# Optimization experiments

Measured on AMD Instinct MI355X. Metric: run time of the kernel, lower is better.

## Reference

```python
import jax, jax.numpy as jnp
import numpy as np

N_HEAD = 16
N_KV_HEAD = 8
HEAD_DIM = 128
N_EMBED = 2048
EPS = 1.1920929e-07  # torch default eps for fp32 rms_norm


def _apply_rotary_emb(x, cos, sin):
    # x: (B, T, H, D); cos/sin: (1, T, 1, D//2)  (nanochat-style half rotation)
    d = x.shape[-1] // 2
    x1, x2 = x[..., :d], x[..., d:]
    y1 = x1 * cos + x2 * sin
    y2 = -x1 * sin + x2 * cos
    return jnp.concatenate([y1, y2], axis=-1).astype(x.dtype)


def _rms_norm(x):
    return x * jax.lax.rsqrt(jnp.mean(jnp.square(x), axis=-1, keepdims=True) + EPS)


def setup_inputs() -> dict:
    key = jax.random.key(0)
    ks = jax.random.split(key, 5)
    B, T = 2, 2048
    kv_dim = N_KV_HEAD * HEAD_DIM
    x = jax.random.normal(ks[0], (B, T, N_EMBED), dtype=jnp.float32)
    w_attn = jax.random.normal(ks[1], (N_EMBED + 2 * kv_dim, N_EMBED), dtype=jnp.float32) * 0.02
    w_proj = jax.random.normal(ks[2], (N_EMBED, N_EMBED), dtype=jnp.float32) * 0.02
    # realistic RoPE tables
    half = HEAD_DIM // 2
    inv_freq = 1.0 / (10000.0 ** (jnp.arange(half, dtype=jnp.float32) / half))
    freqs = jnp.arange(T, dtype=jnp.float32)[:, None] * inv_freq[None, :]  # (T, half)
    cos = jnp.cos(freqs)[None, :, None, :]
    sin = jnp.sin(freqs)[None, :, None, :]
    return {"x": x, "w_attn": w_attn, "w_proj": w_proj, "cos": cos, "sin": sin}


def reference(x, w_attn, w_proj, cos, sin):
    B, T, C = x.shape
    kv_dim = N_KV_HEAD * HEAD_DIM
    qkv = jnp.einsum('btc,oc->bto', x, w_attn)  # (B, T, C + 2*kv_dim)
    q = qkv[..., :C].reshape(B, T, N_HEAD, HEAD_DIM)
    k = qkv[..., C:C + kv_dim].reshape(B, T, N_KV_HEAD, HEAD_DIM)
    v = qkv[..., C + kv_dim:].reshape(B, T, N_KV_HEAD, HEAD_DIM)
    q = _rms_norm(_apply_rotary_emb(q, cos, sin))
    k = _rms_norm(_apply_rotary_emb(k, cos, sin))
    # GQA: repeat kv heads to match query heads
    rep = N_HEAD // N_KV_HEAD
    k = jnp.repeat(k, rep, axis=2)  # (B, T, n_head, D)
    v = jnp.repeat(v, rep, axis=2)
    scale = 1.0 / jnp.sqrt(jnp.float32(HEAD_DIM))
    scores = jnp.einsum('bqhd,bkhd->bhqk', q, k) * scale  # (B, H, T, T)
    causal = jnp.tril(jnp.ones((T, T), dtype=bool))
    scores = jnp.where(causal[None, None], scores, jnp.finfo(scores.dtype).min)
    attn = jax.nn.softmax(scores, axis=-1)
    y = jnp.einsum('bhqk,bkhd->bqhd', attn, v).reshape(B, T, C)
    return jnp.einsum('btc,oc->bto', y, w_proj)
```

## Files before the change

kernel.cpp:

```cpp
#include <hip/hip_runtime.h>

#define B_ 2
#define T_ 2048
#define NH 16
#define NKV 8
#define HD 128
#define C_ 2048
#define KVD (NKV*HD)
#define QKVD (C_ + 2*KVD)
#define NTOK (B_*T_)

typedef __bf16 bf16_t;
typedef __bf16 bf16x2_t __attribute__((ext_vector_type(2)));
typedef __bf16 bf16x4_t __attribute__((ext_vector_type(4)));
typedef __bf16 bf16x8_t __attribute__((ext_vector_type(8)));
typedef float f32x4_t __attribute__((ext_vector_type(4)));
typedef float f32x16_t __attribute__((ext_vector_type(16)));
typedef int i32x4_t __attribute__((ext_vector_type(4)));

__device__ __forceinline__ f32x4_t mfma16(bf16x8_t a, bf16x8_t b, f32x4_t c) {
  return __builtin_amdgcn_mfma_f32_16x16x32_bf16(a, b, c, 0, 0, 0);
}
__device__ __forceinline__ f32x16_t mfma32(bf16x8_t a, bf16x8_t b, f32x16_t c) {
  return __builtin_amdgcn_mfma_f32_32x32x16_bf16(a, b, c, 0, 0, 0);
}
__device__ __forceinline__ f32x16_t zero16() {
  f32x16_t z;
  #pragma unroll
  for (int i = 0; i < 16; i++) z[i] = 0.f;
  return z;
}
__device__ __forceinline__ int pk2(float a, float b) {
  bf16x2_t t; t[0] = (bf16_t)a; t[1] = (bf16_t)b;
  return __builtin_bit_cast(int, t);
}

#define GLDS16(gp, lp) __builtin_amdgcn_global_load_lds( \
    (const __attribute__((address_space(1))) void*)(gp), \
    (__attribute__((address_space(3))) void*)(lp), 16, 0, 0)

__global__ __launch_bounds__(256) void cvt3_kernel(const float* __restrict__ s0, bf16_t* __restrict__ d0,
                                                   const float* __restrict__ s1, bf16_t* __restrict__ d1,
                                                   const float* __restrict__ s2, bf16_t* __restrict__ d2) {
  int bid = blockIdx.x;
  const float* s; bf16_t* d; int off;
  if (bid < 8192)       { s = s0; d = d0; off = bid; }
  else if (bid < 16384) { s = s1; d = d1; off = bid - 8192; }
  else                  { s = s2; d = d2; off = bid - 16384; }
  int i = (off * 256 + threadIdx.x) * 4;
  const float4 v = *(const float4*)(s + i);
  bf16x4_t o;
  o[0] = (bf16_t)v.x; o[1] = (bf16_t)v.y; o[2] = (bf16_t)v.z; o[3] = (bf16_t)v.w;
  *(bf16x4_t*)(d + i) = o;
}

template<int BM>
__global__ __launch_bounds__(512, 1) void gemm_nt2(const bf16_t* __restrict__ A,
                                                   const bf16_t* __restrict__ Bm,
                                                   float* __restrict__ Cf, bf16_t* __restrict__ Cb,
                                                   int M, int N, int K) {
  constexpr int MR = BM / 32;
  constexpr int RA = BM / 64;
  __shared__ __align__(16) bf16_t As[2][BM * 64];
  __shared__ __align__(16) bf16_t Bs[2][256 * 64];
  int tid = threadIdx.x;
  int wave = tid >> 6, lane = tid & 63;
  int quad = lane >> 4, l16 = lane & 15;
  int wm = wave >> 2, wn = wave & 3;
  int gx = gridDim.x;
  int nwg = gx * gridDim.y;
  int flat = blockIdx.y * gx + blockIdx.x;
  int swz = (flat & 7) * (nwg >> 3) + (flat >> 3);
  int bm = (swz / gx) * BM, bn = (swz % gx) * 256;
  int scol = (((tid & 7) ^ ((tid >> 3) & 7))) * 8;
  const bf16_t* pa = A + (size_t)(bm + (tid >> 3)) * K + scol;
  const bf16_t* pb = Bm + (size_t)(bn + (tid >> 3)) * K + scol;
  int ldsrow = (tid >> 3) * 64;

  f32x4_t acc[MR][4];
  #pragma unroll
  for (int i = 0; i < MR; i++)
    #pragma unroll
    for (int j = 0; j < 4; j++) acc[i][j] = (f32x4_t){0.f, 0.f, 0.f, 0.f};

  int nt = K >> 6;
  #pragma unroll
  for (int r = 0; r < RA; r++) GLDS16(pa + (size_t)(r * 64) * K, &As[0][(r * 64 + wave * 8) * 64]);
  #pragma unroll
  for (int r = 0; r < 4; r++)  GLDS16(pb + (size_t)(r * 64) * K, &Bs[0][(r * 64 + wave * 8) * 64]);
  __syncthreads();

  for (int t = 0; t < nt; t++) {
    int cur = t & 1;
    if (t + 1 < nt) {
      int k1 = (t + 1) * 64;
      #pragma unroll
      for (int r = 0; r < RA; r++) GLDS16(pa + (size_t)(r * 64) * K + k1, &As[1 - cur][(r * 64 + wave * 8) * 64]);
      #pragma unroll
      for (int r = 0; r < 4; r++)  GLDS16(pb + (size_t)(r * 64) * K + k1, &Bs[1 - cur][(r * 64 + wave * 8) * 64]);
    }
    bf16x8_t bfr[4][2];
    #pragma unroll
    for (int ni = 0; ni < 4; ni++)
      #pragma unroll
      for (int kh = 0; kh < 2; kh++) {
        int blk = (kh * 4 + quad) ^ (l16 & 7);
        bfr[ni][kh] = *(const bf16x8_t*)&Bs[cur][(wn * 64 + ni * 16 + l16) * 64 + blk * 8];
      }
    #pragma unroll
    for (int g = 0; g < MR / 2; g++) {
      bf16x8_t af[2][2];
      #pragma unroll
      for (int i = 0; i < 2; i++)
        #pragma unroll
        for (int kh = 0; kh < 2; kh++) {
          int blk = (kh * 4 + quad) ^ (l16 & 7);
          af[i][kh] = *(const bf16x8_t*)&As[cur][(wm * (BM / 2) + (g * 2 + i) * 16 + l16) * 64 + blk * 8];
        }
      #pragma unroll
      for (int kh = 0; kh < 2; kh++)
        #pragma unroll
        for (int i = 0; i < 2; i++)
          #pragma unroll
          for (int ni = 0; ni < 4; ni++)
            acc[g * 2 + i][ni] = mfma16(af[i][kh], bfr[ni][kh], acc[g * 2 + i][ni]);
    }
    __syncthreads();
  }
  #pragma unroll
  for (int mi = 0; mi < MR; mi++)
    #pragma unroll
    for (int ni = 0; ni < 4; ni++) {
      int row0 = bm + wm * (BM / 2) + mi * 16 + quad * 4;
      int col  = bn + wn * 64 + ni * 16 + l16;
      if (Cb) {
        #pragma unroll
        for (int r = 0; r < 4; r++)
          Cb[(size_t)(row0 + r) * N + col] = (bf16_t)acc[mi][ni][r];
      } else {
        #pragma unroll
        for (int r = 0; r < 4; r++)
          Cf[(size_t)(row0 + r) * N + col] = acc[mi][ni][r];
      }
    }
}

__global__ __launch_bounds__(256) void rope_norm_kernel(const bf16_t* __restrict__ qkv,
    const float* __restrict__ cosb, const float* __restrict__ sinb,
    bf16_t* __restrict__ qb, bf16_t* __restrict__ kb) {
  int token = blockIdx.y;
  int slot = blockIdx.x * 4 + (threadIdx.x >> 6);
  int lane = threadIdx.x & 63;
  int b = token >> 11, s = token & 2047;
  const bf16_t* row = qkv + (size_t)token * QKVD;
  int base_in = (slot < 16) ? slot * HD : C_ + (slot - 16) * HD;
  float x1 = (float)row[base_in + lane];
  float x2 = (float)row[base_in + 64 + lane];
  float c = cosb[s*64 + lane], sn = sinb[s*64 + lane];
  float y1 = x1*c + x2*sn;
  float y2 = x2*c - x1*sn;
  float ss = y1*y1 + y2*y2;
  ss += __shfl_xor(ss, 1);  ss += __shfl_xor(ss, 2);  ss += __shfl_xor(ss, 4);
  ss += __shfl_xor(ss, 8);  ss += __shfl_xor(ss, 16); ss += __shfl_xor(ss, 32);
  float r = rsqrtf(ss * (1.0f/128.0f) + 1.1920929e-07f);
  bf16_t* dst;
  if (slot < 16) {
    r *= 0.08838834764831845f * 1.4426950408889634f;
    dst = qb + ((size_t)(b*NH + slot) * T_ + s) * HD;
  } else {
    dst = kb + ((size_t)(b*NKV + (slot-16)) * T_ + s) * HD;
  }
  dst[lane]      = (bf16_t)(y1 * r);
  dst[lane + 64] = (bf16_t)(y2 * r);
}

__global__ __launch_bounds__(256) void transpose_v(const bf16_t* __restrict__ qkv,
                                                   bf16_t* __restrict__ vt) {
  __shared__ bf16_t TT[64*136];
  int bk = blockIdx.y;
  int b = bk >> 3, kv = bk & 7;
  int s0 = blockIdx.x * 64;
  int tid = threadIdx.x;
  int row = tid >> 2, c0 = (tid & 3) * 32;
  const bf16_t* src = qkv + (size_t)(b*T_ + s0 + row) * QKVD + C_ + KVD + kv*HD + c0;
  #pragma unroll
  for (int s4 = 0; s4 < 4; s4++)
    *(bf16x8_t*)&TT[row*136 + c0 + s4*8] = *(const bf16x8_t*)(src + s4*8);
  __syncthreads();
  #pragma unroll
  for (int s2 = 0; s2 < 2; s2++) {
    int d = (tid >> 2) + s2*64;
    #pragma unroll
    for (int s = 0; s < 2; s++) {
      int g = (tid & 3) * 8 + s*32;
      bf16x8_t pk;
      #pragma unroll
      for (int e = 0; e < 8; e++) pk[e] = TT[(g + e)*136 + d];
      *(bf16x8_t*)(vt + ((size_t)bk * HD + d) * T_ + s0 + g) = pk;
    }
  }
}

__global__ __launch_bounds__(512, 1) void attn_kernel(const bf16_t* __restrict__ qb,
    const bf16_t* __restrict__ kb, const bf16_t* __restrict__ vt, bf16_t* __restrict__ yb) {
  __shared__ __align__(16) bf16_t Ks[2][2][64*136];
  __shared__ __align__(16) bf16_t Vs[2][2][128*72];
  int L = blockIdx.x;
  int bh = L & 31;
  int qt = 15 - (L >> 5);
  int b = bh >> 4, h = bh & 15, kvh = h >> 1;
  int tid = threadIdx.x;
  int wv = tid >> 6;
  int g  = wv >> 2;
  int sq = wv & 3;
  int lane = tid & 63;
  int l32 = lane & 31, half = lane >> 5;
  int t256 = tid & 255;
  const bf16_t* Qp = qb + (size_t)bh * T_ * HD;
  const bf16_t* Kp = kb + (size_t)(b*NKV + kvh) * T_ * HD;
  const bf16_t* Vt = vt + (size_t)(b*NKV + kvh) * HD * T_;

  int krow = t256 >> 2, kcb = (t256 & 3) * 32;
  int vd = t256 >> 1,  vcb = (t256 & 1) * 32;

  int h0 = qt + 1;
  int kt0 = g * h0;

  int qrow = qt*128 + sq*32 + l32;
  bf16x8_t qf[8];
  #pragma unroll
  for (int kc = 0; kc < 8; kc++)
    qf[kc] = *(const bf16x8_t*)(Qp + (size_t)qrow * HD + kc*16 + half*8);

  float mrow = -1e30f, lrow = 0.f;
  f32x16_t o[4];
  #pragma unroll
  for (int mb = 0; mb < 4; mb++) o[mb] = zero16();

  bf16x8_t kreg[4], vreg[4];
  {
    const bf16_t* srck = Kp + (size_t)(kt0*64 + krow) * HD + kcb;
    const bf16_t* srcv = Vt + (size_t)vd * T_ + kt0*64 + vcb;
    #pragma unroll
    for (int s2 = 0; s2 < 4; s2++) { kreg[s2] = *(const bf16x8_t*)(srck + s2*8);
                                     vreg[s2] = *(const bf16x8_t*)(srcv + s2*8); }
  }
  #pragma unroll
  for (int s2 = 0; s2 < 4; s2++) { *(bf16x8_t*)&Ks[g][0][krow*136 + kcb + s2*8] = kreg[s2];
                                   *(bf16x8_t*)&Vs[g][0][vd*72   + vcb + s2*8] = vreg[s2]; }

  for (int t = 0; t < h0; t++) {
    __syncthreads();
    int cur = t & 1;
    if (t + 1 < h0) {
      int k1 = (kt0 + t + 1) * 64;
      const bf16_t* srck = Kp + (size_t)(k1 + krow) * HD + kcb;
      const bf16_t* srcv = Vt + (size_t)vd * T_ + k1 + vcb;
      #pragma unroll
      for (int s2 = 0; s2 < 4; s2++) { kreg[s2] = *(const bf16x8_t*)(srck + s2*8);
                                       vreg[s2] = *(const bf16x8_t*)(srcv + s2*8); }
    }
    int k0 = (kt0 + t) * 64;
    f32x16_t sacc[2];
    sacc[0] = zero16(); sacc[1] = zero16();
    #pragma unroll
    for (int kc = 0; kc < 8; kc++)
      #pragma unroll
      for (int mb = 0; mb < 2; mb++) {
        bf16x8_t kf = *(const bf16x8_t*)&Ks[g][cur][(mb*32 + l32)*136 + kc*16 + half*8];
        sacc[mb] = mfma32(kf, qf[kc], sacc[mb]);
      }
    if (k0 + 63 > qt*128 + sq*32) {
      #pragma unroll
      for (int mb = 0; mb < 2; mb++)
        #pragma unroll
        for (int r = 0; r < 16; r++) {
          int key = k0 + mb*32 + (r&3) + 8*(r>>2) + 4*half;
          if (key > qrow) sacc[mb][r] = -1e30f;
        }
    }
    float mx = -1e30f;
    #pragma unroll
    for (int mb = 0; mb < 2; mb++)
      #pragma unroll
      for (int r = 0; r < 16; r++) mx = fmaxf(mx, sacc[mb][r]);
    mx = fmaxf(mx, __shfl_xor(mx, 32));
    float mnew = fmaxf(mrow, mx);
    float alpha = exp2f(mrow - mnew);
    mrow = mnew;
    float rs = 0.f;
    #pragma unroll
    for (int mb = 0; mb < 2; mb++)
      #pragma unroll
      for (int r = 0; r < 16; r++) {
        float p = exp2f(sacc[mb][r] - mnew);
        sacc[mb][r] = p;
        rs += p;
      }
    rs += __shfl_xor(rs, 32);
    lrow = lrow * alpha + rs;
    #pragma unroll
    for (int mb = 0; mb < 4; mb++) o[mb] = o[mb] * alpha;
    int P2[2][4][2];
    #pragma unroll
    for (int mb = 0; mb < 2; mb++)
      #pragma unroll
      for (int gg = 0; gg < 4; gg++) {
        P2[mb][gg][0] = pk2(sacc[mb][4*gg+0], sacc[mb][4*gg+1]);
        P2[mb][gg][1] = pk2(sacc[mb][4*gg+2], sacc[mb][4*gg+3]);
      }
    #pragma unroll
    for (int kc = 0; kc < 4; kc++) {
      int mb = kc >> 1, c = kc & 1;
      int o0 = half ? P2[mb][2*c+1][0] : P2[mb][2*c][0];
      int o1 = half ? P2[mb][2*c+1][1] : P2[mb][2*c][1];
      int s0 = half ? P2[mb][2*c][0]   : P2[mb][2*c+1][0];
      int s1 = half ? P2[mb][2*c][1]   : P2[mb][2*c+1][1];
      int r0 = __shfl_xor(s0, 32);
      int r1 = __shfl_xor(s1, 32);
      i32x4_t wvv;
      wvv[0] = half ? r0 : o0;
      wvv[1] = half ? r1 : o1;
      wvv[2] = half ? o0 : r0;
      wvv[3] = half ? o1 : r1;
      bf16x8_t pf = __builtin_bit_cast(bf16x8_t, wvv);
      #pragma unroll
      for (int mbd = 0; mbd < 4; mbd++) {
        bf16x8_t vf = *(const bf16x8_t*)&Vs[g][cur][(mbd*32 + l32)*72 + kc*16 + half*8];
        o[mbd] = mfma32(vf, pf, o[mbd]);
      }
    }
    if (t + 1 < h0) {
      #pragma unroll
      for (int s2 = 0; s2 < 4; s2++) { *(bf16x8_t*)&Ks[g][1-cur][krow*136 + kcb + s2*8] = kreg[s2];
                                       *(bf16x8_t*)&Vs[g][1-cur][vd*72   + vcb + s2*8] = vreg[s2]; }
    }
  }
  __syncthreads();
  float* MG = (float*)Vs;
  int mbase = (sq*64 + lane) * 66;
  if (g == 1) {
    #pragma unroll
    for (int mb = 0; mb < 4; mb++)
      #pragma unroll
      for (int r = 0; r < 16; r++) MG[mbase + mb*16 + r] = o[mb][r];
    MG[mbase + 64] = mrow;
    MG[mbase + 65] = lrow;
  }
  __syncthreads();
  if (g == 0) {
    float m1 = MG[mbase + 64], l1v = MG[mbase + 65];
    float mm = fmaxf(mrow, m1);
    float a0 = exp2f(mrow - mm), a1 = exp2f(m1 - mm);
    float invl = 1.0f / (lrow * a0 + l1v * a1);
    a0 *= invl; a1 *= invl;
    bf16_t* OL = &((bf16_t*)Ks)[sq * 4352];
    #pragma unroll
    for (int mb = 0; mb < 4; mb++)
      #pragma unroll
      for (int rr = 0; rr < 4; rr++) {
        bf16x4_t pk;
        #pragma unroll
        for (int jj = 0; jj < 4; jj++)
          pk[jj] = (bf16_t)(o[mb][rr*4+jj] * a0 + MG[mbase + mb*16 + rr*4 + jj] * a1);
        *(bf16x4_t*)&OL[l32*136 + mb*32 + rr*8 + half*4] = pk;
      }
    int tok = qt*128 + sq*32 + l32;
    bf16_t* dst = yb + ((size_t)(b*T_ + tok) * NH + h) * HD + half*64;
    #pragma unroll
    for (int jj = 0; jj < 8; jj++)
      *(bf16x8_t*)(dst + jj*8) = *(const bf16x8_t*)&OL[l32*136 + half*64 + jj*8];
  }
}

extern "C" void kernel_launch(void* const* d_in, const int* in_sizes, int n_in,
                              void* d_out, int out_size, void* d_ws, size_t ws_size,
                              hipStream_t stream) {
  const float* x      = (const float*)d_in[0];
  const float* w_attn = (const float*)d_in[1];
  const float* w_proj = (const float*)d_in[2];
  const float* cosb   = (const float*)d_in[3];
  const float* sinb   = (const float*)d_in[4];
  float* out = (float*)d_out;

  bf16_t* xb   = (bf16_t*)d_ws;
  bf16_t* wab  = xb + 8388608;
  bf16_t* wpb  = wab + 8388608;
  bf16_t* qkvb = wpb + 4194304;
  bf16_t* qb   = qkvb + 16777216;
  bf16_t* kb   = qb + 8388608;
  bf16_t* vt   = kb + 4194304;
  bf16_t* yb   = vt + 4194304;

  cvt3_kernel<<<20480, 256, 0, stream>>>(x, xb, w_attn, wab, w_proj, wpb);

  gemm_nt2<256><<<dim3(16, 16), 512, 0, stream>>>(xb, wab, nullptr, qkvb, NTOK, QKVD, C_);

  rope_norm_kernel<<<dim3(6, 4096), 256, 0, stream>>>(qkvb, cosb, sinb, qb, kb);
  transpose_v<<<dim3(32, 16), 256, 0, stream>>>(qkvb, vt);

  attn_kernel<<<512, 512, 0, stream>>>(qb, kb, vt, yb);

  gemm_nt2<128><<<dim3(8, 32), 512, 0, stream>>>(yb, wpb, out, nullptr, NTOK, C_, C_);
}
```

Before: 321.7 us.

## Add phase-interleaved QKV GEMM with split global-to-LDS staging and priority hints

```diff
diff --git a/kernel.cpp b/kernel.cpp
--- a/kernel.cpp
+++ b/kernel.cpp
@@ -38,6 +38,8 @@
 #define GLDS16(gp, lp) __builtin_amdgcn_global_load_lds( \
     (const __attribute__((address_space(1))) void*)(gp), \
     (__attribute__((address_space(3))) void*)(lp), 16, 0, 0)
+
+#define CFENCE() asm volatile("" ::: "memory")
 
 __global__ __launch_bounds__(256) void cvt3_kernel(const float* __restrict__ s0, bf16_t* __restrict__ d0,
                                                    const float* __restrict__ s1, bf16_t* __restrict__ d1,
@@ -52,6 +54,100 @@
   bf16x4_t o;
   o[0] = (bf16_t)v.x; o[1] = (bf16_t)v.y; o[2] = (bf16_t)v.z; o[3] = (bf16_t)v.w;
   *(bf16x4_t*)(d + i) = o;
+}
+
+__global__ __launch_bounds__(512, 1) void gemm8p(const bf16_t* __restrict__ A,
+                                                 const bf16_t* __restrict__ Bm,
+                                                 bf16_t* __restrict__ Cb,
+                                                 int M, int N, int K) {
+  __shared__ __align__(16) bf16_t As[2][256 * 64];
+  __shared__ __align__(16) bf16_t Bs[2][256 * 64];
+  int tid = threadIdx.x;
+  int wave = tid >> 6, lane = tid & 63;
+  int quad = lane >> 4, l16 = lane & 15;
+  int wm = wave >> 2, wn = wave & 3;
+  int gx = gridDim.x, nwg = gx * gridDim.y;
+  int flat = blockIdx.y * gx + blockIdx.x;
+  int swz = (flat & 7) * (nwg >> 3) + (flat >> 3);
+  int bm = (swz / gx) * 256, bn = (swz % gx) * 256;
+  int scol = ((tid & 7) ^ ((tid >> 3) & 7)) * 8;
+  int srow = tid >> 3;
+  const bf16_t* pa = A + (size_t)(bm + srow) * K + scol;
+  const bf16_t* pb = Bm + (size_t)(bn + srow) * K + scol;
+
+#define STAGE_A8(buf, tile, h) { \
+    GLDS16(pa + (size_t)((h)*128 + 0) * K + (size_t)(tile)*64, &As[buf][((h)*128 + 0 + wave*8)*64]); \
+    GLDS16(pa + (size_t)((h)*128 + 64) * K + (size_t)(tile)*64, &As[buf][((h)*128 + 64 + wave*8)*64]); }
+#define STAGE_B8(buf, tile, h) { \
+    GLDS16(pb + (size_t)((h)*128 + 0) * K + (size_t)(tile)*64, &Bs[buf][((h)*128 + 0 + wave*8)*64]); \
+    GLDS16(pb + (size_t)((h)*128 + 64) * K + (size_t)(tile)*64, &Bs[buf][((h)*128 + 64 + wave*8)*64]); }
+
+  f32x4_t acc[8][4];
+  #pragma unroll
+  for (int i = 0; i < 8; i++)
+    #pragma unroll
+    for (int j = 0; j < 4; j++) acc[i][j] = (f32x4_t){0.f, 0.f, 0.f, 0.f};
+
+  int nt = K >> 6;
+  STAGE_A8(0, 0, 0); STAGE_A8(0, 0, 1); STAGE_B8(0, 0, 0); STAGE_B8(0, 0, 1);
+  STAGE_B8(1, 1, 0); STAGE_B8(1, 1, 1);
+  asm volatile("s_waitcnt vmcnt(4)" ::: "memory");
+  CFENCE(); __builtin_amdgcn_s_barrier(); CFENCE();
+
+  for (int s = 0; s < nt; ++s) {
+    int b = s & 1;
+    bf16x8_t bfr[4][2];
+    #pragma unroll
+    for (int jph = 0; jph < 4; ++jph) {
+      if (jph == 0) {
+        #pragma unroll
+        for (int ni = 0; ni < 4; ni++)
+          #pragma unroll
+          for (int kh = 0; kh < 2; kh++)
+            bfr[ni][kh] = *(const bf16x8_t*)&Bs[b][(wn*64 + ni*16 + l16)*64 + (((kh*4 + quad) ^ (l16 & 7))*8)];
+      }
+      bf16x8_t af[2][2];
+      #pragma unroll
+      for (int i = 0; i < 2; i++)
+        #pragma unroll
+        for (int kh = 0; kh < 2; kh++)
+          af[i][kh] = *(const bf16x8_t*)&As[b][(wm*128 + (jph*2 + i)*16 + l16)*64 + (((kh*4 + quad) ^ (l16 & 7))*8)];
+      if (jph == 0) { if (s + 1 < nt) STAGE_A8(1 - b, s + 1, 0); }
+      if (jph == 1) { if (s + 1 < nt) STAGE_A8(1 - b, s + 1, 1); }
+      if (jph == 2) { if (s + 2 < nt) STAGE_B8(b, s + 2, 0); }
+      if (jph == 3) {
+        if (s + 2 < nt) {
+          STAGE_B8(b, s + 2, 1);
+          asm volatile("s_waitcnt vmcnt(4)" ::: "memory");
+        } else {
+          asm volatile("s_waitcnt vmcnt(0)" ::: "memory");
+        }
+      }
+      CFENCE(); __builtin_amdgcn_s_barrier(); CFENCE();
+      __builtin_amdgcn_s_setprio(1);
+      #pragma unroll
+      for (int kh = 0; kh < 2; kh++)
+        #pragma unroll
+        for (int i = 0; i < 2; i++)
+          #pragma unroll
+          for (int ni = 0; ni < 4; ni++)
+            acc[jph*2 + i][ni] = mfma16(af[i][kh], bfr[ni][kh], acc[jph*2 + i][ni]);
+      __builtin_amdgcn_s_setprio(0);
+      CFENCE(); __builtin_amdgcn_s_barrier(); CFENCE();
+    }
+  }
+  #pragma unroll
+  for (int mi = 0; mi < 8; mi++)
+    #pragma unroll
+    for (int ni = 0; ni < 4; ni++) {
+      int row0 = bm + wm*128 + mi*16 + quad*4;
+      int col  = bn + wn*64 + ni*16 + l16;
+      #pragma unroll
+      for (int r = 0; r < 4; r++)
+        Cb[(size_t)(row0 + r) * N + col] = (bf16_t)acc[mi][ni][r];
+    }
+#undef STAGE_A8
+#undef STAGE_B8
 }
 
 template<int BM>
@@ -75,7 +171,6 @@
   int scol = (((tid & 7) ^ ((tid >> 3) & 7))) * 8;
   const bf16_t* pa = A + (size_t)(bm + (tid >> 3)) * K + scol;
   const bf16_t* pb = Bm + (size_t)(bn + (tid >> 3)) * K + scol;
-  int ldsrow = (tid >> 3) * 64;
 
   f32x4_t acc[MR][4];
   #pragma unroll
@@ -394,7 +489,7 @@
 
   cvt3_kernel<<<20480, 256, 0, stream>>>(x, xb, w_attn, wab, w_proj, wpb);
 
-  gemm_nt2<256><<<dim3(16, 16), 512, 0, stream>>>(xb, wab, nullptr, qkvb, NTOK, QKVD, C_);
+  gemm8p<<<dim3(16, 16), 512, 0, stream>>>(xb, wab, qkvb, NTOK, QKVD, C_);
 
   rope_norm_kernel<<<dim3(6, 4096), 256, 0, stream>>>(qkvb, cosb, sinb, qb, kb);
   transpose_v<<<dim3(32, 16), 256, 0, stream>>>(qkvb, vt);
```

Measured after the change: 322.3 us. No clear change (+0.2%).
